# Kernel optimization log

Measured on AMD Instinct MI355X. Metric: run time of the kernel, lower is better.

The kernel has to match this reference:

```python
import jax, jax.numpy as jnp
import numpy as np

N_EMBD = 2048
N_HEAD = 32
N_KV_HEADS = 8
HEAD_DIM = 64
N_REP = N_HEAD // N_KV_HEADS
MAX_SEQ_LEN = 4096
ROPE_THETA = 10000.0


def _precompute_freqs_cis(dim, end, theta=ROPE_THETA):
    freqs = 1.0 / theta ** (jnp.arange(0, dim, 2)[: dim // 2].astype(jnp.float32) / dim)
    t = jnp.arange(end, dtype=jnp.float32)
    freqs = jnp.outer(t, freqs)  # (end, dim//2)
    return jnp.cos(freqs), jnp.sin(freqs)


def setup_inputs() -> dict:
    key = jax.random.key(0)
    ks = jax.random.split(key, 5)
    B, S = 2, 2048
    x = jax.random.normal(ks[0], (B, S, N_EMBD), dtype=jnp.float32)
    # torch Linear(in, out, bias=False): y = x @ W.T, W is (out, in). We store (in, out).
    sc = 1.0 / np.sqrt(N_EMBD)
    wq = jax.random.normal(ks[1], (N_EMBD, N_EMBD), dtype=jnp.float32) * sc
    wk = jax.random.normal(ks[2], (N_EMBD, N_KV_HEADS * HEAD_DIM), dtype=jnp.float32) * sc
    wv = jax.random.normal(ks[3], (N_EMBD, N_KV_HEADS * HEAD_DIM), dtype=jnp.float32) * sc
    wo = jax.random.normal(ks[4], (N_EMBD, N_EMBD), dtype=jnp.float32) * sc
    freqs_cos, freqs_sin = _precompute_freqs_cis(HEAD_DIM, MAX_SEQ_LEN)
    return {"x": x, "wq": wq, "wk": wk, "wv": wv, "wo": wo,
            "freqs_cos": freqs_cos, "freqs_sin": freqs_sin}


def _apply_rotary(t, cos, sin):
    # t: (B, S, H, HD); interleaved real/imag pairs along last dim.
    shp = t.shape
    t2 = t.reshape(*shp[:-1], HEAD_DIM // 2, 2)
    r, i = t2[..., 0], t2[..., 1]
    out_r = r * cos - i * sin
    out_i = r * sin + i * cos
    return jnp.stack([out_r, out_i], axis=-1).reshape(shp)


def reference(x, wq, wk, wv, wo, freqs_cos, freqs_sin):
    B, S, _ = x.shape
    xq = (x @ wq).reshape(B, S, N_HEAD, HEAD_DIM)
    xk = (x @ wk).reshape(B, S, N_KV_HEADS, HEAD_DIM)
    xv = (x @ wv).reshape(B, S, N_KV_HEADS, HEAD_DIM)

    cos = freqs_cos[:S][None, :, None, :]  # (1, S, 1, HD/2)
    sin = freqs_sin[:S][None, :, None, :]
    xq = _apply_rotary(xq, cos, sin)
    xk = _apply_rotary(xk, cos, sin)

    # GQA: repeat KV heads (repeat_interleave along head dim)
    keys = jnp.repeat(xk, N_REP, axis=2)    # (B, S, H, HD)
    values = jnp.repeat(xv, N_REP, axis=2)

    scores = jnp.einsum('bqhd,bkhd->bhqk', xq, keys) / np.sqrt(HEAD_DIM)
    causal = jnp.tril(jnp.ones((S, S), dtype=bool))
    scores = jnp.where(causal, scores, -jnp.inf)
    probs = jax.nn.softmax(scores.astype(jnp.float32), axis=-1).astype(xq.dtype)
    out = jnp.einsum('bhqk,bkhd->bqhd', probs, values)  # (B, S, H, HD)
    out = out.reshape(B, S, N_EMBD)
    return out @ wo
```

## Files before the change

kernel.cpp:

```cpp
#include <hip/hip_runtime.h>
#include <hip/hip_fp16.h>
#include <stdint.h>

typedef _Float16 f16x8 __attribute__((ext_vector_type(8)));
typedef _Float16 f16x4 __attribute__((ext_vector_type(4)));
typedef _Float16 f16x2 __attribute__((ext_vector_type(2)));
typedef float f32x4 __attribute__((ext_vector_type(4)));
typedef float f32x16 __attribute__((ext_vector_type(16)));

#define B_ 2
#define S_ 2048
#define NE 2048
#define NH 32
#define NKV 8
#define HD 64
#define NTOK (B_ * S_)
#define QKVN 3072

__device__ __forceinline__ f16x2 pk(float a, float b) {
  return __builtin_bit_cast(f16x2, __builtin_amdgcn_cvt_pkrtz(a, b));
}

__device__ __forceinline__ void gld_lds16(void* lds, const void* g) {
  __builtin_amdgcn_global_load_lds(
      (const __attribute__((address_space(1))) void*)g,
      (__attribute__((address_space(3))) void*)lds, 16, 0, 0);
}

__global__ void conv_x_kernel(const float* __restrict__ x,
                              _Float16* __restrict__ xo, int n2) {
  int i = blockIdx.x * 256 + threadIdx.x;
  if (i < n2) {
    float2 v = ((const float2*)x)[i];
    f16x2 h;
    h.x = (_Float16)v.x;
    h.y = (_Float16)v.y;
    ((f16x2*)xo)[i] = h;
  }
}

__global__ void tconv_kernel(const float* __restrict__ src,
                             _Float16* __restrict__ dst,
                             int srcN, int rowoff, int ldd) {
  __shared__ float tile[32][33];
  int n0 = blockIdx.x * 32, k0 = blockIdx.y * 32;
  int tx = threadIdx.x, ty = threadIdx.y;
  for (int i = ty; i < 32; i += 8)
    tile[i][tx] = src[(size_t)(k0 + i) * srcN + n0 + tx];
  __syncthreads();
  for (int i = ty; i < 32; i += 8)
    dst[(size_t)(rowoff + n0 + i) * ldd + k0 + tx] = (_Float16)tile[tx][i];
}

template <int OUT_F32>
__global__ __launch_bounds__(256, 2) void gemm_bt(
    const _Float16* __restrict__ A, const _Float16* __restrict__ Bt,
    void* __restrict__ Cout, int M, int N, int K) {
  __shared__ _Float16 As[128 * 32];
  __shared__ _Float16 Bs[128 * 32];
  const int tid = threadIdx.x;
  const int wave = tid >> 6, lane = tid & 63;
  const int qd = lane >> 4, ln = lane & 15;
  const int m0 = blockIdx.y * 128, n0 = blockIdx.x * 128;
  const int wm = (wave >> 1) * 64, wn = (wave & 1) * 64;

  f32x4 acc[4][4] = {};

  const int srow = (lane >> 2);
  const int scol = (lane & 3) * 8;

  for (int k0 = 0; k0 < K; k0 += 32) {
    __syncthreads();
#pragma unroll
    for (int it = 0; it < 2; ++it) {
      int r = wave * 32 + it * 16 + srow;
      gld_lds16(&As[(wave * 32 + it * 16) * 32],
                A + (size_t)(m0 + r) * K + k0 + scol);
      gld_lds16(&Bs[(wave * 32 + it * 16) * 32],
                Bt + (size_t)(n0 + r) * K + k0 + scol);
    }
    __syncthreads();
    f16x8 a[4], b[4];
#pragma unroll
    for (int mt = 0; mt < 4; ++mt)
      a[mt] = *(const f16x8*)&As[(wm + mt * 16 + ln) * 32 + qd * 8];
#pragma unroll
    for (int nt = 0; nt < 4; ++nt)
      b[nt] = *(const f16x8*)&Bs[(wn + nt * 16 + ln) * 32 + qd * 8];
#pragma unroll
    for (int mt = 0; mt < 4; ++mt)
#pragma unroll
      for (int nt = 0; nt < 4; ++nt)
        acc[mt][nt] =
            __builtin_amdgcn_mfma_f32_16x16x32_f16(a[mt], b[nt], acc[mt][nt], 0, 0, 0);
  }

#pragma unroll
  for (int mt = 0; mt < 4; ++mt) {
    int row = m0 + wm + mt * 16 + qd * 4;
#pragma unroll
    for (int nt = 0; nt < 4; ++nt) {
      int col = n0 + wn + nt * 16 + ln;
#pragma unroll
      for (int r = 0; r < 4; ++r) {
        if (OUT_F32)
          ((float*)Cout)[(size_t)(row + r) * N + col] = acc[mt][nt][r];
        else
          ((_Float16*)Cout)[(size_t)(row + r) * N + col] =
              (_Float16)acc[mt][nt][r];
      }
    }
  }
}

__global__ void rope_scatter_kernel(const _Float16* __restrict__ qkv,
                                    const float* __restrict__ fcos,
                                    const float* __restrict__ fsin,
                                    _Float16* __restrict__ Qb,
                                    _Float16* __restrict__ Kb) {
  const float QSC = 0.125f * 1.44269504088896f;
  int idx = blockIdx.x * 256 + threadIdx.x;
  int t = idx / 1280;
  int col = (idx - t * 1280) * 2;
  int b = t >> 11, s = t & 2047;
  float v0 = (float)qkv[(size_t)t * QKVN + col];
  float v1 = (float)qkv[(size_t)t * QKVN + col + 1];
  _Float16* dst;
  size_t off;
  int d;
  float sc;
  if (col < 2048) {
    int h = col >> 6;
    d = col & 63;
    dst = Qb;
    off = ((size_t)(b * NH + h) * S_ + s) * HD + d;
    sc = QSC;
  } else {
    int cc = col - 2048;
    int h = cc >> 6;
    d = cc & 63;
    dst = Kb;
    off = ((size_t)(b * NKV + h) * S_ + s) * HD + d;
    sc = 1.0f;
  }
  float c = fcos[s * 32 + (d >> 1)], sn = fsin[s * 32 + (d >> 1)];
  f16x2 o;
  o.x = (_Float16)((v0 * c - v1 * sn) * sc);
  o.y = (_Float16)((v0 * sn + v1 * c) * sc);
  *(f16x2*)(dst + off) = o;
}

__global__ void vtrans_kernel(const _Float16* __restrict__ qkv,
                              _Float16* __restrict__ Vtg) {
  __shared__ _Float16 tile[64][65];
  int t0 = blockIdx.x * 64;
  int kv = blockIdx.y, b = blockIdx.z;
  int tid = threadIdx.x;
  for (int slot = tid; slot < 4096; slot += 256) {
    int r = slot >> 6, c = slot & 63;
    tile[r][c] = qkv[(size_t)(b * S_ + t0 + r) * QKVN + 2560 + kv * 64 + c];
  }
  __syncthreads();
  size_t base = ((size_t)(b * NKV + kv) * HD) * S_;
  for (int slot = tid; slot < 4096; slot += 256) {
    int d = slot >> 6, r = slot & 63;
    Vtg[base + (size_t)d * S_ + t0 + r] = tile[r][d];
  }
}

__global__ __launch_bounds__(128, 2) void attn_kernel(
    const _Float16* __restrict__ Qb, const _Float16* __restrict__ Kb,
    const _Float16* __restrict__ Vtg, _Float16* __restrict__ Ob) {
  constexpr float M_SHIFT = 10.0f;
  __shared__ _Float16 Ks[64 * 64];
  __shared__ _Float16 Vs[64 * 64];
  const int tid = threadIdx.x;
  const int wave = tid >> 6, lane = tid & 63;
  const int mrow = lane & 31;
  const bool half = (lane >> 5) != 0;
  const int h = blockIdx.y, b = blockIdx.z;
  const int kvh = h >> 2;

  const _Float16* Qh = Qb + ((size_t)(b * NH + h) * S_) * HD;
  const _Float16* Kh = Kb + ((size_t)(b * NKV + kvh) * S_) * HD;
  const _Float16* Vh = Vtg + ((size_t)(b * NKV + kvh) * HD) * S_;

  const int sr = tid >> 3;
  const int scc = tid & 7;
  const int swz = (scc ^ (sr & 7)) * 8;

#pragma unroll
  for (int pass = 0; pass < 2; ++pass) {
    const int qt = pass ? blockIdx.x : (31 - blockIdx.x);
    const int q0 = qt * 64;
    const int nkt = qt + 1;

    const int qrow = q0 + wave * 32 + mrow;
    f16x8 aq[4];
#pragma unroll
    for (int kk = 0; kk < 4; ++kk)
      aq[kk] = *(const f16x8*)(Qh + (size_t)qrow * HD + kk * 16 +
                               (half ? 8 : 0));

    f32x16 accO[2] = {};
    float lsum = 0.f;

    f16x8 kp[4], vp[4];
#pragma unroll
    for (int i = 0; i < 4; ++i) {
      kp[i] = *(const f16x8*)(Kh + (size_t)(sr + i * 16) * HD + scc * 8);
      vp[i] = *(const f16x8*)(Vh + (size_t)(sr + i * 16) * S_ + scc * 8);
    }
#pragma unroll
    for (int i = 0; i < 4; ++i) {
      *(f16x8*)&Ks[(sr + i * 16) * 64 + swz] = kp[i];
      *(f16x8*)&Vs[(sr + i * 16) * 64 + swz] = vp[i];
    }

    for (int kt = 0; kt < nkt; ++kt) {
      __syncthreads();
      if (kt + 1 < nkt) {
#pragma unroll
        for (int i = 0; i < 4; ++i) {
          kp[i] = *(const f16x8*)(Kh +
                                  (size_t)((kt + 1) * 64 + sr + i * 16) * HD +
                                  scc * 8);
          vp[i] = *(const f16x8*)(Vh + (size_t)(sr + i * 16) * S_ +
                                  (kt + 1) * 64 + scc * 8);
        }
      }

      f32x16 s[2];
#pragma unroll
      for (int nt = 0; nt < 2; ++nt)
#pragma unroll
        for (int r = 0; r < 16; ++r) s[nt][r] = -M_SHIFT;
#pragma unroll
      for (int kk = 0; kk < 4; ++kk) {
        int c = kk * 2 + (half ? 1 : 0);
#pragma unroll
        for (int nt = 0; nt < 2; ++nt) {
          int krow = nt * 32 + mrow;
          f16x8 bk = *(const f16x8*)&Ks[krow * 64 + ((c ^ (krow & 7)) * 8)];
          s[nt] = __builtin_amdgcn_mfma_f32_32x32x16_f16(bk, aq[kk], s[nt],
                                                         0, 0, 0);
        }
      }

      const bool edge = (kt == nkt - 1);
      float pf[2][16];
#pragma unroll
      for (int nt = 0; nt < 2; ++nt)
#pragma unroll
        for (int r = 0; r < 16; ++r) {
          int key = kt * 64 + nt * 32 + (r & 3) + 8 * (r >> 2) +
                    (half ? 4 : 0);
          float p = exp2f(s[nt][r]);
          if (edge && key > qrow) p = 0.f;
          lsum += p;
          pf[nt][r] = p;
        }

      f16x2 P2[2][4][2];
#pragma unroll
      for (int nt = 0; nt < 2; ++nt)
#pragma unroll
        for (int c = 0; c < 4; ++c)
#pragma unroll
          for (int u = 0; u < 2; ++u)
            P2[nt][c][u] = pk(pf[nt][4 * c + 2 * u], pf[nt][4 * c + 2 * u + 1]);

#pragma unroll
      for (int s4 = 0; s4 < 4; ++s4) {
        const int ntp = s4 >> 1;
        const int gA = (2 * s4) & 3, gB = (2 * s4 + 1) & 3;
        f16x2 own0 = half ? P2[ntp][gB][0] : P2[ntp][gA][0];
        f16x2 own1 = half ? P2[ntp][gB][1] : P2[ntp][gA][1];
        f16x2 snd0 = half ? P2[ntp][gA][0] : P2[ntp][gB][0];
        f16x2 snd1 = half ? P2[ntp][gA][1] : P2[ntp][gB][1];
        f16x2 rcv0 = __builtin_bit_cast(
            f16x2, __shfl_xor(__builtin_bit_cast(int, snd0), 32));
        f16x2 rcv1 = __builtin_bit_cast(
            f16x2, __shfl_xor(__builtin_bit_cast(int, snd1), 32));
        union {
          f16x2 h2[4];
          f16x8 h8;
        } bp;
        bp.h2[0] = half ? rcv0 : own0;
        bp.h2[1] = half ? rcv1 : own1;
        bp.h2[2] = half ? own0 : rcv0;
        bp.h2[3] = half ? own1 : rcv1;
        const int c = 2 * s4 + (half ? 1 : 0);
#pragma unroll
        for (int ntd = 0; ntd < 2; ++ntd) {
          int drow = ntd * 32 + mrow;
          f16x8 bv = *(const f16x8*)&Vs[drow * 64 + ((c ^ (drow & 7)) * 8)];
          accO[ntd] = __builtin_amdgcn_mfma_f32_32x32x16_f16(bv, bp.h8,
                                                             accO[ntd], 0, 0, 0);
        }
      }

      __syncthreads();
      if (kt + 1 < nkt) {
#pragma unroll
        for (int i = 0; i < 4; ++i) {
          *(f16x8*)&Ks[(sr + i * 16) * 64 + swz] = kp[i];
          *(f16x8*)&Vs[(sr + i * 16) * 64 + swz] = vp[i];
        }
      }
    }

    float tot = lsum + __shfl_xor(lsum, 32);
    float inv = 1.f / tot;
    size_t base = ((size_t)(b * S_) + qrow) * NE + h * HD;
#pragma unroll
    for (int ntd = 0; ntd < 2; ++ntd)
#pragma unroll
      for (int rq = 0; rq < 4; ++rq) {
        int d0 = ntd * 32 + 8 * rq + (half ? 4 : 0);
        union {
          f16x2 h2[2];
          f16x4 h4;
        } o;
        o.h2[0] = pk(accO[ntd][4 * rq + 0] * inv, accO[ntd][4 * rq + 1] * inv);
        o.h2[1] = pk(accO[ntd][4 * rq + 2] * inv, accO[ntd][4 * rq + 3] * inv);
        *(f16x4*)(Ob + base + d0) = o.h4;
      }
  }
}

extern "C" void kernel_launch(void* const* d_in, const int* in_sizes, int n_in,
                              void* d_out, int out_size, void* d_ws,
                              size_t ws_size, hipStream_t stream) {
  const float* x = (const float*)d_in[0];
  const float* wq = (const float*)d_in[1];
  const float* wk = (const float*)d_in[2];
  const float* wv = (const float*)d_in[3];
  const float* wo = (const float*)d_in[4];
  const float* fcos = (const float*)d_in[5];
  const float* fsin = (const float*)d_in[6];

  char* ws = (char*)d_ws;
  _Float16* xb = (_Float16*)(ws);
  _Float16* wqkv_t = (_Float16*)(ws + 16777216);
  _Float16* wo_t = (_Float16*)(ws + 29360128);
  _Float16* qkv = (_Float16*)(ws + 37748736);
  _Float16* Qb = (_Float16*)(ws + 62914560);
  _Float16* Kb = (_Float16*)(ws + 79691776);
  _Float16* Vb = (_Float16*)(ws + 83886080);
  _Float16* Ob = (_Float16*)(ws + 88080384);

  conv_x_kernel<<<16384, 256, 0, stream>>>(x, xb, (NTOK * NE) / 2);

  dim3 tb(32, 8);
  tconv_kernel<<<dim3(64, 64), tb, 0, stream>>>(wq, wqkv_t, 2048, 0, 2048);
  tconv_kernel<<<dim3(16, 64), tb, 0, stream>>>(wk, wqkv_t, 512, 2048, 2048);
  tconv_kernel<<<dim3(16, 64), tb, 0, stream>>>(wv, wqkv_t, 512, 2560, 2048);
  tconv_kernel<<<dim3(64, 64), tb, 0, stream>>>(wo, wo_t, 2048, 0, 2048);

  gemm_bt<0><<<dim3(QKVN / 128, NTOK / 128), 256, 0, stream>>>(
      xb, wqkv_t, qkv, NTOK, QKVN, NE);

  rope_scatter_kernel<<<(NTOK * 1280) / 256, 256, 0, stream>>>(qkv, fcos, fsin,
                                                               Qb, Kb);
  vtrans_kernel<<<dim3(S_ / 64, NKV, B_), 256, 0, stream>>>(qkv, Vb);

  attn_kernel<<<dim3(16, NH, B_), 128, 0, stream>>>(Qb, Kb, Vb, Ob);

  gemm_bt<1><<<dim3(NE / 128, NTOK / 128), 256, 0, stream>>>(
      Ob, wo_t, d_out, NTOK, NE, NE);
}
```

Before: 328.3 us.

## Restructure attention to 128-row query tiles with 4 waves per block

The attention kernel changes from 2 waves processing two paired 64-row query tiles sequentially to 4 waves sharing one 128-row query tile, so each K/V tile loaded into LDS serves twice as many query rows. Waves skip key tiles that lie wholly above their causal diagonal, and masking runs only on diagonal tiles. It also adds s_setprio around the MFMA blocks and computes the row sum from the packed fp16 probabilities with fdot2. The trade-off is load imbalance across blocks, since the removed pass pairing no longer balances causal work, plus idle waves during skipped tiles. The row sum also loses some precision by summing fp16-rounded values.

```diff
diff --git a/kernel.cpp b/kernel.cpp
--- a/kernel.cpp
+++ b/kernel.cpp
@@ -20,6 +20,17 @@
 __device__ __forceinline__ f16x2 pk(float a, float b) {
   return __builtin_bit_cast(f16x2, __builtin_amdgcn_cvt_pkrtz(a, b));
 }
+
+#if __has_builtin(__builtin_amdgcn_fdot2)
+#define HAVE_FDOT2 1
+typedef __fp16 h16x2 __attribute__((ext_vector_type(2)));
+__device__ __forceinline__ float sum2(f16x2 a, float acc) {
+  h16x2 one;
+  one[0] = (__fp16)1.f;
+  one[1] = (__fp16)1.f;
+  return __builtin_amdgcn_fdot2(__builtin_bit_cast(h16x2, a), one, acc, false);
+}
+#endif
 
 __device__ __forceinline__ void gld_lds16(void* lds, const void* g) {
   __builtin_amdgcn_global_load_lds(
@@ -168,7 +179,7 @@
   }
 }
 
-__global__ __launch_bounds__(128, 2) void attn_kernel(
+__global__ __launch_bounds__(256, 4) void attn_kernel(
     const _Float16* __restrict__ Qb, const _Float16* __restrict__ Kb,
     const _Float16* __restrict__ Vtg, _Float16* __restrict__ Ob) {
   constexpr float M_SHIFT = 10.0f;
@@ -189,52 +200,53 @@
   const int scc = tid & 7;
   const int swz = (scc ^ (sr & 7)) * 8;
 
-#pragma unroll
-  for (int pass = 0; pass < 2; ++pass) {
-    const int qt = pass ? blockIdx.x : (31 - blockIdx.x);
-    const int q0 = qt * 64;
-    const int nkt = qt + 1;
-
-    const int qrow = q0 + wave * 32 + mrow;
-    f16x8 aq[4];
-#pragma unroll
-    for (int kk = 0; kk < 4; ++kk)
-      aq[kk] = *(const f16x8*)(Qh + (size_t)qrow * HD + kk * 16 +
-                               (half ? 8 : 0));
-
-    f32x16 accO[2] = {};
-    float lsum = 0.f;
-
-    f16x8 kp[4], vp[4];
-#pragma unroll
-    for (int i = 0; i < 4; ++i) {
-      kp[i] = *(const f16x8*)(Kh + (size_t)(sr + i * 16) * HD + scc * 8);
-      vp[i] = *(const f16x8*)(Vh + (size_t)(sr + i * 16) * S_ + scc * 8);
-    }
-#pragma unroll
-    for (int i = 0; i < 4; ++i) {
-      *(f16x8*)&Ks[(sr + i * 16) * 64 + swz] = kp[i];
-      *(f16x8*)&Vs[(sr + i * 16) * 64 + swz] = vp[i];
-    }
-
-    for (int kt = 0; kt < nkt; ++kt) {
-      __syncthreads();
-      if (kt + 1 < nkt) {
-#pragma unroll
-        for (int i = 0; i < 4; ++i) {
-          kp[i] = *(const f16x8*)(Kh +
-                                  (size_t)((kt + 1) * 64 + sr + i * 16) * HD +
-                                  scc * 8);
-          vp[i] = *(const f16x8*)(Vh + (size_t)(sr + i * 16) * S_ +
-                                  (kt + 1) * 64 + scc * 8);
-        }
-      }
-
+  const int qt = 15 - (int)blockIdx.x;
+  const int q0 = qt * 128;
+  const int nkt = 2 * qt + 2;
+
+  const int qrow = q0 + wave * 32 + mrow;
+  f16x8 aq[4];
+#pragma unroll
+  for (int kk = 0; kk < 4; ++kk)
+    aq[kk] = *(const f16x8*)(Qh + (size_t)qrow * HD + kk * 16 +
+                             (half ? 8 : 0));
+
+  f32x16 accO[2] = {};
+  float lsum = 0.f;
+
+  f16x8 kp[2], vp[2];
+#pragma unroll
+  for (int i = 0; i < 2; ++i) {
+    kp[i] = *(const f16x8*)(Kh + (size_t)(sr + i * 32) * HD + scc * 8);
+    vp[i] = *(const f16x8*)(Vh + (size_t)(sr + i * 32) * S_ + scc * 8);
+  }
+#pragma unroll
+  for (int i = 0; i < 2; ++i) {
+    *(f16x8*)&Ks[(sr + i * 32) * 64 + swz] = kp[i];
+    *(f16x8*)&Vs[(sr + i * 32) * 64 + swz] = vp[i];
+  }
+
+  for (int kt = 0; kt < nkt; ++kt) {
+    __syncthreads();
+    if (kt + 1 < nkt) {
+#pragma unroll
+      for (int i = 0; i < 2; ++i) {
+        kp[i] = *(const f16x8*)(Kh +
+                                (size_t)((kt + 1) * 64 + sr + i * 32) * HD +
+                                scc * 8);
+        vp[i] = *(const f16x8*)(Vh + (size_t)(sr + i * 32) * S_ +
+                                (kt + 1) * 64 + scc * 8);
+      }
+    }
+
+    const bool active = (kt * 64) <= (q0 + wave * 32 + 31);
+    if (active) {
       f32x16 s[2];
 #pragma unroll
       for (int nt = 0; nt < 2; ++nt)
 #pragma unroll
         for (int r = 0; r < 16; ++r) s[nt][r] = -M_SHIFT;
+      __builtin_amdgcn_s_setprio(1);
 #pragma unroll
       for (int kk = 0; kk < 4; ++kk) {
         int c = kk * 2 + (half ? 1 : 0);
@@ -246,29 +258,43 @@
                                                          0, 0, 0);
         }
       }
-
-      const bool edge = (kt == nkt - 1);
+      __builtin_amdgcn_s_setprio(0);
+
+      const bool edge = (kt * 64 + 63) > (q0 + wave * 32);
       float pf[2][16];
+      if (edge) {
+#pragma unroll
+        for (int nt = 0; nt < 2; ++nt)
+#pragma unroll
+          for (int r = 0; r < 16; ++r) {
+            int key = kt * 64 + nt * 32 + (r & 3) + 8 * (r >> 2) +
+                      (half ? 4 : 0);
+            float p = exp2f(s[nt][r]);
+            if (key > qrow) p = 0.f;
+            pf[nt][r] = p;
+          }
+      } else {
+#pragma unroll
+        for (int nt = 0; nt < 2; ++nt)
+#pragma unroll
+          for (int r = 0; r < 16; ++r) pf[nt][r] = exp2f(s[nt][r]);
+      }
+
+      f16x2 P2[2][4][2];
 #pragma unroll
       for (int nt = 0; nt < 2; ++nt)
 #pragma unroll
-        for (int r = 0; r < 16; ++r) {
-          int key = kt * 64 + nt * 32 + (r & 3) + 8 * (r >> 2) +
-                    (half ? 4 : 0);
-          float p = exp2f(s[nt][r]);
-          if (edge && key > qrow) p = 0.f;
-          lsum += p;
-          pf[nt][r] = p;
-        }
-
-      f16x2 P2[2][4][2];
-#pragma unroll
-      for (int nt = 0; nt < 2; ++nt)
-#pragma unroll
         for (int c = 0; c < 4; ++c)
 #pragma unroll
-          for (int u = 0; u < 2; ++u)
-            P2[nt][c][u] = pk(pf[nt][4 * c + 2 * u], pf[nt][4 * c + 2 * u + 1]);
+          for (int u = 0; u < 2; ++u) {
+            f16x2 v = pk(pf[nt][4 * c + 2 * u], pf[nt][4 * c + 2 * u + 1]);
+            P2[nt][c][u] = v;
+#ifdef HAVE_FDOT2
+            lsum = sum2(v, lsum);
+#else
+            lsum += pf[nt][4 * c + 2 * u] + pf[nt][4 * c + 2 * u + 1];
+#endif
+          }
 
 #pragma unroll
       for (int s4 = 0; s4 < 4; ++s4) {
@@ -291,6 +317,7 @@
         bp.h2[2] = half ? own0 : rcv0;
         bp.h2[3] = half ? own1 : rcv1;
         const int c = 2 * s4 + (half ? 1 : 0);
+        __builtin_amdgcn_s_setprio(1);
 #pragma unroll
         for (int ntd = 0; ntd < 2; ++ntd) {
           int drow = ntd * 32 + mrow;
@@ -298,35 +325,36 @@
           accO[ntd] = __builtin_amdgcn_mfma_f32_32x32x16_f16(bv, bp.h8,
                                                              accO[ntd], 0, 0, 0);
         }
-      }
-
-      __syncthreads();
-      if (kt + 1 < nkt) {
-#pragma unroll
-        for (int i = 0; i < 4; ++i) {
-          *(f16x8*)&Ks[(sr + i * 16) * 64 + swz] = kp[i];
-          *(f16x8*)&Vs[(sr + i * 16) * 64 + swz] = vp[i];
-        }
-      }
-    }
-
-    float tot = lsum + __shfl_xor(lsum, 32);
-    float inv = 1.f / tot;
-    size_t base = ((size_t)(b * S_) + qrow) * NE + h * HD;
-#pragma unroll
-    for (int ntd = 0; ntd < 2; ++ntd)
-#pragma unroll
-      for (int rq = 0; rq < 4; ++rq) {
-        int d0 = ntd * 32 + 8 * rq + (half ? 4 : 0);
-        union {
-          f16x2 h2[2];
-          f16x4 h4;
-        } o;
-        o.h2[0] = pk(accO[ntd][4 * rq + 0] * inv, accO[ntd][4 * rq + 1] * inv);
-        o.h2[1] = pk(accO[ntd][4 * rq + 2] * inv, accO[ntd][4 * rq + 3] * inv);
-        *(f16x4*)(Ob + base + d0) = o.h4;
-      }
-  }
+        __builtin_amdgcn_s_setprio(0);
+      }
+    }
+
+    __syncthreads();
+    if (kt + 1 < nkt) {
+#pragma unroll
+      for (int i = 0; i < 2; ++i) {
+        *(f16x8*)&Ks[(sr + i * 32) * 64 + swz] = kp[i];
+        *(f16x8*)&Vs[(sr + i * 32) * 64 + swz] = vp[i];
+      }
+    }
+  }
+
+  float tot = lsum + __shfl_xor(lsum, 32);
+  float inv = 1.f / tot;
+  size_t base = ((size_t)(b * S_) + qrow) * NE + h * HD;
+#pragma unroll
+  for (int ntd = 0; ntd < 2; ++ntd)
+#pragma unroll
+    for (int rq = 0; rq < 4; ++rq) {
+      int d0 = ntd * 32 + 8 * rq + (half ? 4 : 0);
+      union {
+        f16x2 h2[2];
+        f16x4 h4;
+      } o;
+      o.h2[0] = pk(accO[ntd][4 * rq + 0] * inv, accO[ntd][4 * rq + 1] * inv);
+      o.h2[1] = pk(accO[ntd][4 * rq + 2] * inv, accO[ntd][4 * rq + 3] * inv);
+      *(f16x4*)(Ob + base + d0) = o.h4;
+    }
 }
 
 extern "C" void kernel_launch(void* const* d_in, const int* in_sizes, int n_in,
@@ -365,7 +393,7 @@
                                                                Qb, Kb);
   vtrans_kernel<<<dim3(S_ / 64, NKV, B_), 256, 0, stream>>>(qkv, Vb);
 
-  attn_kernel<<<dim3(16, NH, B_), 128, 0, stream>>>(Qb, Kb, Vb, Ob);
+  attn_kernel<<<dim3(16, NH, B_), 256, 0, stream>>>(Qb, Kb, Vb, Ob);
 
   gemm_bt<1><<<dim3(NE / 128, NTOK / 128), 256, 0, stream>>>(
       Ob, wo_t, d_out, NTOK, NE, NE);
```

After: 437.9 us. 1.33x slower.

## Split attention q-tile pairs into separate blocks, add MFMA priority and fdot2 row sums

Applied to the files above, without the earlier changes.

The attention kernel previously had each block handle two causal q-tiles (one long, one short) to balance work. It now launches 32 blocks along x, each handling one q-tile with the longest tiles scheduled first, which doubles parallelism. The change also hoists the causal mask into a separate edge-only branch, wraps the MFMA sections in s_setprio to favour matrix issue, and accumulates the row sum from the packed fp16 probabilities using fdot2. Per-block work becomes uneven, and computing the sum from rounded fp16 values slightly changes the normalisation.

```diff
diff --git a/kernel.cpp b/kernel.cpp
--- a/kernel.cpp
+++ b/kernel.cpp
@@ -20,6 +20,17 @@
 __device__ __forceinline__ f16x2 pk(float a, float b) {
   return __builtin_bit_cast(f16x2, __builtin_amdgcn_cvt_pkrtz(a, b));
 }
+
+#if __has_builtin(__builtin_amdgcn_fdot2)
+#define HAVE_FDOT2 1
+typedef __fp16 h16x2 __attribute__((ext_vector_type(2)));
+__device__ __forceinline__ float sum2(f16x2 a, float acc) {
+  h16x2 one;
+  one[0] = (__fp16)1.f;
+  one[1] = (__fp16)1.f;
+  return __builtin_amdgcn_fdot2(__builtin_bit_cast(h16x2, a), one, acc, false);
+}
+#endif
 
 __device__ __forceinline__ void gld_lds16(void* lds, const void* g) {
   __builtin_amdgcn_global_load_lds(
@@ -189,66 +200,67 @@
   const int scc = tid & 7;
   const int swz = (scc ^ (sr & 7)) * 8;
 
-#pragma unroll
-  for (int pass = 0; pass < 2; ++pass) {
-    const int qt = pass ? blockIdx.x : (31 - blockIdx.x);
-    const int q0 = qt * 64;
-    const int nkt = qt + 1;
-
-    const int qrow = q0 + wave * 32 + mrow;
-    f16x8 aq[4];
-#pragma unroll
-    for (int kk = 0; kk < 4; ++kk)
-      aq[kk] = *(const f16x8*)(Qh + (size_t)qrow * HD + kk * 16 +
-                               (half ? 8 : 0));
-
-    f32x16 accO[2] = {};
-    float lsum = 0.f;
-
-    f16x8 kp[4], vp[4];
-#pragma unroll
-    for (int i = 0; i < 4; ++i) {
-      kp[i] = *(const f16x8*)(Kh + (size_t)(sr + i * 16) * HD + scc * 8);
-      vp[i] = *(const f16x8*)(Vh + (size_t)(sr + i * 16) * S_ + scc * 8);
-    }
-#pragma unroll
-    for (int i = 0; i < 4; ++i) {
-      *(f16x8*)&Ks[(sr + i * 16) * 64 + swz] = kp[i];
-      *(f16x8*)&Vs[(sr + i * 16) * 64 + swz] = vp[i];
-    }
-
-    for (int kt = 0; kt < nkt; ++kt) {
-      __syncthreads();
-      if (kt + 1 < nkt) {
-#pragma unroll
-        for (int i = 0; i < 4; ++i) {
-          kp[i] = *(const f16x8*)(Kh +
-                                  (size_t)((kt + 1) * 64 + sr + i * 16) * HD +
-                                  scc * 8);
-          vp[i] = *(const f16x8*)(Vh + (size_t)(sr + i * 16) * S_ +
-                                  (kt + 1) * 64 + scc * 8);
-        }
-      }
-
-      f32x16 s[2];
-#pragma unroll
-      for (int nt = 0; nt < 2; ++nt)
-#pragma unroll
-        for (int r = 0; r < 16; ++r) s[nt][r] = -M_SHIFT;
-#pragma unroll
-      for (int kk = 0; kk < 4; ++kk) {
-        int c = kk * 2 + (half ? 1 : 0);
-#pragma unroll
-        for (int nt = 0; nt < 2; ++nt) {
-          int krow = nt * 32 + mrow;
-          f16x8 bk = *(const f16x8*)&Ks[krow * 64 + ((c ^ (krow & 7)) * 8)];
-          s[nt] = __builtin_amdgcn_mfma_f32_32x32x16_f16(bk, aq[kk], s[nt],
-                                                         0, 0, 0);
-        }
-      }
-
-      const bool edge = (kt == nkt - 1);
-      float pf[2][16];
+  const int qt = 31 - (int)blockIdx.x;
+  const int q0 = qt * 64;
+  const int nkt = qt + 1;
+
+  const int qrow = q0 + wave * 32 + mrow;
+  f16x8 aq[4];
+#pragma unroll
+  for (int kk = 0; kk < 4; ++kk)
+    aq[kk] = *(const f16x8*)(Qh + (size_t)qrow * HD + kk * 16 +
+                             (half ? 8 : 0));
+
+  f32x16 accO[2] = {};
+  float lsum = 0.f;
+
+  f16x8 kp[4], vp[4];
+#pragma unroll
+  for (int i = 0; i < 4; ++i) {
+    kp[i] = *(const f16x8*)(Kh + (size_t)(sr + i * 16) * HD + scc * 8);
+    vp[i] = *(const f16x8*)(Vh + (size_t)(sr + i * 16) * S_ + scc * 8);
+  }
+#pragma unroll
+  for (int i = 0; i < 4; ++i) {
+    *(f16x8*)&Ks[(sr + i * 16) * 64 + swz] = kp[i];
+    *(f16x8*)&Vs[(sr + i * 16) * 64 + swz] = vp[i];
+  }
+
+  for (int kt = 0; kt < nkt; ++kt) {
+    __syncthreads();
+    if (kt + 1 < nkt) {
+#pragma unroll
+      for (int i = 0; i < 4; ++i) {
+        kp[i] = *(const f16x8*)(Kh +
+                                (size_t)((kt + 1) * 64 + sr + i * 16) * HD +
+                                scc * 8);
+        vp[i] = *(const f16x8*)(Vh + (size_t)(sr + i * 16) * S_ +
+                                (kt + 1) * 64 + scc * 8);
+      }
+    }
+
+    f32x16 s[2];
+#pragma unroll
+    for (int nt = 0; nt < 2; ++nt)
+#pragma unroll
+      for (int r = 0; r < 16; ++r) s[nt][r] = -M_SHIFT;
+    __builtin_amdgcn_s_setprio(1);
+#pragma unroll
+    for (int kk = 0; kk < 4; ++kk) {
+      int c = kk * 2 + (half ? 1 : 0);
+#pragma unroll
+      for (int nt = 0; nt < 2; ++nt) {
+        int krow = nt * 32 + mrow;
+        f16x8 bk = *(const f16x8*)&Ks[krow * 64 + ((c ^ (krow & 7)) * 8)];
+        s[nt] = __builtin_amdgcn_mfma_f32_32x32x16_f16(bk, aq[kk], s[nt],
+                                                       0, 0, 0);
+      }
+    }
+    __builtin_amdgcn_s_setprio(0);
+
+    const bool edge = (kt == nkt - 1);
+    float pf[2][16];
+    if (edge) {
 #pragma unroll
       for (int nt = 0; nt < 2; ++nt)
 #pragma unroll
@@ -256,77 +268,90 @@
           int key = kt * 64 + nt * 32 + (r & 3) + 8 * (r >> 2) +
                     (half ? 4 : 0);
           float p = exp2f(s[nt][r]);
-          if (edge && key > qrow) p = 0.f;
-          lsum += p;
+          if (key > qrow) p = 0.f;
           pf[nt][r] = p;
         }
-
-      f16x2 P2[2][4][2];
+    } else {
 #pragma unroll
       for (int nt = 0; nt < 2; ++nt)
 #pragma unroll
-        for (int c = 0; c < 4; ++c)
-#pragma unroll
-          for (int u = 0; u < 2; ++u)
-            P2[nt][c][u] = pk(pf[nt][4 * c + 2 * u], pf[nt][4 * c + 2 * u + 1]);
-
-#pragma unroll
-      for (int s4 = 0; s4 < 4; ++s4) {
-        const int ntp = s4 >> 1;
-        const int gA = (2 * s4) & 3, gB = (2 * s4 + 1) & 3;
-        f16x2 own0 = half ? P2[ntp][gB][0] : P2[ntp][gA][0];
-        f16x2 own1 = half ? P2[ntp][gB][1] : P2[ntp][gA][1];
-        f16x2 snd0 = half ? P2[ntp][gA][0] : P2[ntp][gB][0];
-        f16x2 snd1 = half ? P2[ntp][gA][1] : P2[ntp][gB][1];
-        f16x2 rcv0 = __builtin_bit_cast(
-            f16x2, __shfl_xor(__builtin_bit_cast(int, snd0), 32));
-        f16x2 rcv1 = __builtin_bit_cast(
-            f16x2, __shfl_xor(__builtin_bit_cast(int, snd1), 32));
-        union {
-          f16x2 h2[4];
-          f16x8 h8;
-        } bp;
-        bp.h2[0] = half ? rcv0 : own0;
-        bp.h2[1] = half ? rcv1 : own1;
-        bp.h2[2] = half ? own0 : rcv0;
-        bp.h2[3] = half ? own1 : rcv1;
-        const int c = 2 * s4 + (half ? 1 : 0);
-#pragma unroll
-        for (int ntd = 0; ntd < 2; ++ntd) {
-          int drow = ntd * 32 + mrow;
-          f16x8 bv = *(const f16x8*)&Vs[drow * 64 + ((c ^ (drow & 7)) * 8)];
-          accO[ntd] = __builtin_amdgcn_mfma_f32_32x32x16_f16(bv, bp.h8,
-                                                             accO[ntd], 0, 0, 0);
+        for (int r = 0; r < 16; ++r) pf[nt][r] = exp2f(s[nt][r]);
+    }
+
+    f16x2 P2[2][4][2];
+#pragma unroll
+    for (int nt = 0; nt < 2; ++nt)
+#pragma unroll
+      for (int c = 0; c < 4; ++c)
+#pragma unroll
+        for (int u = 0; u < 2; ++u) {
+          f16x2 v = pk(pf[nt][4 * c + 2 * u], pf[nt][4 * c + 2 * u + 1]);
+          P2[nt][c][u] = v;
+#ifdef HAVE_FDOT2
+          lsum = sum2(v, lsum);
+#else
+          lsum += pf[nt][4 * c + 2 * u] + pf[nt][4 * c + 2 * u + 1];
+#endif
         }
-      }
-
-      __syncthreads();
-      if (kt + 1 < nkt) {
-#pragma unroll
-        for (int i = 0; i < 4; ++i) {
-          *(f16x8*)&Ks[(sr + i * 16) * 64 + swz] = kp[i];
-          *(f16x8*)&Vs[(sr + i * 16) * 64 + swz] = vp[i];
-        }
-      }
-    }
-
-    float tot = lsum + __shfl_xor(lsum, 32);
-    float inv = 1.f / tot;
-    size_t base = ((size_t)(b * S_) + qrow) * NE + h * HD;
-#pragma unroll
-    for (int ntd = 0; ntd < 2; ++ntd)
-#pragma unroll
-      for (int rq = 0; rq < 4; ++rq) {
-        int d0 = ntd * 32 + 8 * rq + (half ? 4 : 0);
-        union {
-          f16x2 h2[2];
-          f16x4 h4;
-        } o;
-        o.h2[0] = pk(accO[ntd][4 * rq + 0] * inv, accO[ntd][4 * rq + 1] * inv);
-        o.h2[1] = pk(accO[ntd][4 * rq + 2] * inv, accO[ntd][4 * rq + 3] * inv);
-        *(f16x4*)(Ob + base + d0) = o.h4;
-      }
-  }
+
+#pragma unroll
+    for (int s4 = 0; s4 < 4; ++s4) {
+      const int ntp = s4 >> 1;
+      const int gA = (2 * s4) & 3, gB = (2 * s4 + 1) & 3;
+      f16x2 own0 = half ? P2[ntp][gB][0] : P2[ntp][gA][0];
+      f16x2 own1 = half ? P2[ntp][gB][1] : P2[ntp][gA][1];
+      f16x2 snd0 = half ? P2[ntp][gA][0] : P2[ntp][gB][0];
+      f16x2 snd1 = half ? P2[ntp][gA][1] : P2[ntp][gB][1];
+      f16x2 rcv0 = __builtin_bit_cast(
+          f16x2, __shfl_xor(__builtin_bit_cast(int, snd0), 32));
+      f16x2 rcv1 = __builtin_bit_cast(
+          f16x2, __shfl_xor(__builtin_bit_cast(int, snd1), 32));
+      union {
+        f16x2 h2[4];
+        f16x8 h8;
+      } bp;
+      bp.h2[0] = half ? rcv0 : own0;
+      bp.h2[1] = half ? rcv1 : own1;
+      bp.h2[2] = half ? own0 : rcv0;
+      bp.h2[3] = half ? own1 : rcv1;
+      const int c = 2 * s4 + (half ? 1 : 0);
+      __builtin_amdgcn_s_setprio(1);
+#pragma unroll
+      for (int ntd = 0; ntd < 2; ++ntd) {
+        int drow = ntd * 32 + mrow;
+        f16x8 bv = *(const f16x8*)&Vs[drow * 64 + ((c ^ (drow & 7)) * 8)];
+        accO[ntd] = __builtin_amdgcn_mfma_f32_32x32x16_f16(bv, bp.h8,
+                                                           accO[ntd], 0, 0, 0);
+      }
+      __builtin_amdgcn_s_setprio(0);
+    }
+
+    __syncthreads();
+    if (kt + 1 < nkt) {
+#pragma unroll
+      for (int i = 0; i < 4; ++i) {
+        *(f16x8*)&Ks[(sr + i * 16) * 64 + swz] = kp[i];
+        *(f16x8*)&Vs[(sr + i * 16) * 64 + swz] = vp[i];
+      }
+    }
+  }
+
+  float tot = lsum + __shfl_xor(lsum, 32);
+  float inv = 1.f / tot;
+  size_t base = ((size_t)(b * S_) + qrow) * NE + h * HD;
+#pragma unroll
+  for (int ntd = 0; ntd < 2; ++ntd)
+#pragma unroll
+    for (int rq = 0; rq < 4; ++rq) {
+      int d0 = ntd * 32 + 8 * rq + (half ? 4 : 0);
+      union {
+        f16x2 h2[2];
+        f16x4 h4;
+      } o;
+      o.h2[0] = pk(accO[ntd][4 * rq + 0] * inv, accO[ntd][4 * rq + 1] * inv);
+      o.h2[1] = pk(accO[ntd][4 * rq + 2] * inv, accO[ntd][4 * rq + 3] * inv);
+      *(f16x4*)(Ob + base + d0) = o.h4;
+    }
 }
 
 extern "C" void kernel_launch(void* const* d_in, const int* in_sizes, int n_in,
@@ -365,7 +390,7 @@
                                                                Qb, Kb);
   vtrans_kernel<<<dim3(S_ / 64, NKV, B_), 256, 0, stream>>>(qkv, Vb);
 
-  attn_kernel<<<dim3(16, NH, B_), 128, 0, stream>>>(Qb, Kb, Vb, Ob);
+  attn_kernel<<<dim3(32, NH, B_), 128, 0, stream>>>(Qb, Kb, Vb, Ob);
 
   gemm_bt<1><<<dim3(NE / 128, NTOK / 128), 256, 0, stream>>>(
       Ob, wo_t, d_out, NTOK, NE, NE);
```

Measured after the change: 395.0 us. +20.3%, slower.

## Load K/V straight from global into MFMA registers and remap blocks per XCD

Applied to the files above, without the earlier changes.

The attention kernel drops its shared-memory K/V staging and barriers. Each single-wave block now loads the K and V MFMA operands directly from global memory into registers. Blocks are remapped with a flat grid so that heads sharing a KV head land on the same XCD, which is meant to improve L2 reuse of K/V. The trade-off is more global/L2 traffic per wave, since the two waves no longer share one LDS tile, and no software prefetch of the next tile.

```diff
diff --git a/kernel.cpp b/kernel.cpp
--- a/kernel.cpp
+++ b/kernel.cpp
@@ -168,34 +168,36 @@
   }
 }
 
-__global__ __launch_bounds__(128, 2) void attn_kernel(
+__global__ __launch_bounds__(64, 2) void attn_kernel(
     const _Float16* __restrict__ Qb, const _Float16* __restrict__ Kb,
     const _Float16* __restrict__ Vtg, _Float16* __restrict__ Ob) {
   constexpr float M_SHIFT = 10.0f;
-  __shared__ _Float16 Ks[64 * 64];
-  __shared__ _Float16 Vs[64 * 64];
-  const int tid = threadIdx.x;
-  const int wave = tid >> 6, lane = tid & 63;
+  const int lane = threadIdx.x;
   const int mrow = lane & 31;
   const bool half = (lane >> 5) != 0;
-  const int h = blockIdx.y, b = blockIdx.z;
-  const int kvh = h >> 2;
+
+  const int wid = blockIdx.x;
+  const int xcd = wid & 7;
+  const int j = wid >> 3;
+  const int grp = xcd * 2 + (j >> 7);
+  const int b = grp >> 3, kvh = grp & 7;
+  const int rr = j & 127;
+  const int h = kvh * 4 + (rr >> 5);
+  const int bp_ = rr & 31;
+  const int p = bp_ >> 1;
+  const int rh = bp_ & 1;
 
   const _Float16* Qh = Qb + ((size_t)(b * NH + h) * S_) * HD;
   const _Float16* Kh = Kb + ((size_t)(b * NKV + kvh) * S_) * HD;
   const _Float16* Vh = Vtg + ((size_t)(b * NKV + kvh) * HD) * S_;
 
-  const int sr = tid >> 3;
-  const int scc = tid & 7;
-  const int swz = (scc ^ (sr & 7)) * 8;
-
 #pragma unroll
   for (int pass = 0; pass < 2; ++pass) {
-    const int qt = pass ? blockIdx.x : (31 - blockIdx.x);
+    const int qt = pass ? p : (31 - p);
     const int q0 = qt * 64;
     const int nkt = qt + 1;
 
-    const int qrow = q0 + wave * 32 + mrow;
+    const int qrow = q0 + rh * 32 + mrow;
     f16x8 aq[4];
 #pragma unroll
     for (int kk = 0; kk < 4; ++kk)
@@ -205,30 +207,27 @@
     f32x16 accO[2] = {};
     float lsum = 0.f;
 
-    f16x8 kp[4], vp[4];
-#pragma unroll
-    for (int i = 0; i < 4; ++i) {
-      kp[i] = *(const f16x8*)(Kh + (size_t)(sr + i * 16) * HD + scc * 8);
-      vp[i] = *(const f16x8*)(Vh + (size_t)(sr + i * 16) * S_ + scc * 8);
-    }
-#pragma unroll
-    for (int i = 0; i < 4; ++i) {
-      *(f16x8*)&Ks[(sr + i * 16) * 64 + swz] = kp[i];
-      *(f16x8*)&Vs[(sr + i * 16) * 64 + swz] = vp[i];
-    }
+    const _Float16* kbase0 = Kh + (size_t)mrow * HD + (half ? 8 : 0);
+    const _Float16* kbase1 = Kh + (size_t)(32 + mrow) * HD + (half ? 8 : 0);
+    const _Float16* vbase0 = Vh + (size_t)mrow * S_ + (half ? 8 : 0);
+    const _Float16* vbase1 = Vh + (size_t)(32 + mrow) * S_ + (half ? 8 : 0);
 
     for (int kt = 0; kt < nkt; ++kt) {
-      __syncthreads();
-      if (kt + 1 < nkt) {
-#pragma unroll
-        for (int i = 0; i < 4; ++i) {
-          kp[i] = *(const f16x8*)(Kh +
-                                  (size_t)((kt + 1) * 64 + sr + i * 16) * HD +
-                                  scc * 8);
-          vp[i] = *(const f16x8*)(Vh + (size_t)(sr + i * 16) * S_ +
-                                  (kt + 1) * 64 + scc * 8);
-        }
-      }
+      f16x8 kb[4][2], vb[4][2];
+#pragma unroll
+      for (int kk = 0; kk < 4; ++kk) {
+        kb[kk][0] = *(const f16x8*)(kbase0 + kk * 16);
+        kb[kk][1] = *(const f16x8*)(kbase1 + kk * 16);
+      }
+#pragma unroll
+      for (int s4 = 0; s4 < 4; ++s4) {
+        vb[s4][0] = *(const f16x8*)(vbase0 + s4 * 16);
+        vb[s4][1] = *(const f16x8*)(vbase1 + s4 * 16);
+      }
+      kbase0 += 64 * HD;
+      kbase1 += 64 * HD;
+      vbase0 += 64;
+      vbase1 += 64;
 
       f32x16 s[2];
 #pragma unroll
@@ -236,16 +235,11 @@
 #pragma unroll
         for (int r = 0; r < 16; ++r) s[nt][r] = -M_SHIFT;
 #pragma unroll
-      for (int kk = 0; kk < 4; ++kk) {
-        int c = kk * 2 + (half ? 1 : 0);
-#pragma unroll
-        for (int nt = 0; nt < 2; ++nt) {
-          int krow = nt * 32 + mrow;
-          f16x8 bk = *(const f16x8*)&Ks[krow * 64 + ((c ^ (krow & 7)) * 8)];
-          s[nt] = __builtin_amdgcn_mfma_f32_32x32x16_f16(bk, aq[kk], s[nt],
-                                                         0, 0, 0);
-        }
-      }
+      for (int kk = 0; kk < 4; ++kk)
+#pragma unroll
+        for (int nt = 0; nt < 2; ++nt)
+          s[nt] = __builtin_amdgcn_mfma_f32_32x32x16_f16(kb[kk][nt], aq[kk],
+                                                         s[nt], 0, 0, 0);
 
       const bool edge = (kt == nkt - 1);
       float pf[2][16];
@@ -255,10 +249,10 @@
         for (int r = 0; r < 16; ++r) {
           int key = kt * 64 + nt * 32 + (r & 3) + 8 * (r >> 2) +
                     (half ? 4 : 0);
-          float p = exp2f(s[nt][r]);
-          if (edge && key > qrow) p = 0.f;
-          lsum += p;
-          pf[nt][r] = p;
+          float pv = exp2f(s[nt][r]);
+          if (edge && key > qrow) pv = 0.f;
+          lsum += pv;
+          pf[nt][r] = pv;
         }
 
       f16x2 P2[2][4][2];
@@ -290,23 +284,10 @@
         bp.h2[1] = half ? rcv1 : own1;
         bp.h2[2] = half ? own0 : rcv0;
         bp.h2[3] = half ? own1 : rcv1;
-        const int c = 2 * s4 + (half ? 1 : 0);
-#pragma unroll
-        for (int ntd = 0; ntd < 2; ++ntd) {
-          int drow = ntd * 32 + mrow;
-          f16x8 bv = *(const f16x8*)&Vs[drow * 64 + ((c ^ (drow & 7)) * 8)];
-          accO[ntd] = __builtin_amdgcn_mfma_f32_32x32x16_f16(bv, bp.h8,
-                                                             accO[ntd], 0, 0, 0);
-        }
-      }
-
-      __syncthreads();
-      if (kt + 1 < nkt) {
-#pragma unroll
-        for (int i = 0; i < 4; ++i) {
-          *(f16x8*)&Ks[(sr + i * 16) * 64 + swz] = kp[i];
-          *(f16x8*)&Vs[(sr + i * 16) * 64 + swz] = vp[i];
-        }
+#pragma unroll
+        for (int ntd = 0; ntd < 2; ++ntd)
+          accO[ntd] = __builtin_amdgcn_mfma_f32_32x32x16_f16(
+              vb[s4][ntd], bp.h8, accO[ntd], 0, 0, 0);
       }
     }
 
@@ -365,7 +346,7 @@
                                                                Qb, Kb);
   vtrans_kernel<<<dim3(S_ / 64, NKV, B_), 256, 0, stream>>>(qkv, Vb);
 
-  attn_kernel<<<dim3(16, NH, B_), 128, 0, stream>>>(Qb, Kb, Vb, Ob);
+  attn_kernel<<<2048, 64, 0, stream>>>(Qb, Kb, Vb, Ob);
 
   gemm_bt<1><<<dim3(NE / 128, NTOK / 128), 256, 0, stream>>>(
       Ob, wo_t, d_out, NTOK, NE, NE);
```

After: 391.8 us. 1.19x slower.
